# Optimization experiments

Hardware: AMD Instinct MI355X
Metric: run time of the kernel (lower is better)

The kernel has to match this reference:

```python
import jax, jax.numpy as jnp
import numpy as np

EMBED = 768
HEADS = 12
HEAD_DIM = EMBED // HEADS
HIDDEN = 4 * EMBED


def layer_norm(x, gamma, beta, eps=1e-5):
    mu = jnp.mean(x, axis=-1, keepdims=True)
    var = jnp.var(x, axis=-1, keepdims=True)
    return (x - mu) * jax.lax.rsqrt(var + eps) * gamma + beta


def setup_inputs() -> dict:
    key = jax.random.key(0)
    ks = jax.random.split(key, 10)
    B, N, C = 64, 577, EMBED
    s_in = 1.0 / np.sqrt(C)
    s_hid = 1.0 / np.sqrt(HIDDEN)
    return {
        "x": jax.random.normal(ks[0], (B, N, C), jnp.float32),
        "ln1_g": jnp.ones((C,), jnp.float32),
        "ln1_b": jnp.zeros((C,), jnp.float32),
        "w_qkv": jax.random.normal(ks[1], (C, 3 * C), jnp.float32) * s_in,  # no bias (qkv_bias=False)
        "w_proj": jax.random.normal(ks[2], (C, C), jnp.float32) * s_in,
        "b_proj": jnp.zeros((C,), jnp.float32),
        "ln2_g": jnp.ones((C,), jnp.float32),
        "ln2_b": jnp.zeros((C,), jnp.float32),
        "w_fc1": jax.random.normal(ks[3], (C, HIDDEN), jnp.float32) * s_in,
        "b_fc1": jnp.zeros((HIDDEN,), jnp.float32),
        "w_fc2": jax.random.normal(ks[4], (HIDDEN, C), jnp.float32) * s_hid,
        "b_fc2": jnp.zeros((C,), jnp.float32),
    }


def reference(x, ln1_g, ln1_b, w_qkv, w_proj, b_proj, ln2_g, ln2_b, w_fc1, b_fc1, w_fc2, b_fc2):
    B, N, C = x.shape
    # --- attention branch (pre-norm) ---
    h = layer_norm(x, ln1_g, ln1_b)
    qkv = (h @ w_qkv).reshape(B, N, 3, HEADS, HEAD_DIM)
    q = jnp.transpose(qkv[:, :, 0], (0, 2, 1, 3))  # [B,H,N,D]
    k = jnp.transpose(qkv[:, :, 1], (0, 2, 1, 3))
    v = jnp.transpose(qkv[:, :, 2], (0, 2, 1, 3))
    scale = HEAD_DIM ** -0.5
    att = jax.nn.softmax(jnp.einsum("bhnd,bhmd->bhnm", q, k) * scale, axis=-1)
    o = jnp.einsum("bhnm,bhmd->bhnd", att, v)
    o = jnp.transpose(o, (0, 2, 1, 3)).reshape(B, N, C)
    x = x + (o @ w_proj + b_proj)
    # --- MLP branch (pre-norm) ---
    h = layer_norm(x, ln2_g, ln2_b)
    h = jax.nn.gelu(h @ w_fc1 + b_fc1, approximate=False)
    x = x + (h @ w_fc2 + b_fc2)
    return x
```

## Files before the change

kernel.cpp:

```cpp
#include <hip/hip_runtime.h>
#include <hip/hip_bf16.h>
#include <math.h>

using bf16 = __hip_bfloat16;
typedef __attribute__((ext_vector_type(8))) short short8;
typedef __attribute__((ext_vector_type(4))) float f32x4;

#define NSEQ   577
#define NBATCH 64
#define NTOK   36928
#define MPAD   37120
#define NHEADS 12
#define HDIM   64
#define NP     640
#define CEMB   768
#define CHID   3072
#define NBH    (NBATCH*NHEADS)

__device__ __forceinline__ bf16 f2bf(float v){ return __float2bfloat16(v); }

__device__ __forceinline__ float gelu_f(float x) {
    float x3 = x * x * x;
    float y = 1.5957691216057308f * (x + 0.044715f * x3);
    float e = __expf(y);
    float t = 1.0f - 2.0f / (e + 1.0f);
    return 0.5f * x * (1.0f + t);
}

#define GLOAD_LDS16(gaddr, laddr) \
  __builtin_amdgcn_global_load_lds((__attribute__((address_space(1))) const void*)(gaddr), \
                                   (__attribute__((address_space(3))) void*)(laddr), 16, 0, 0)

__global__ __launch_bounds__(256) void transpose_w(const float* __restrict__ src,
                                                   bf16* __restrict__ dst, int R, int C) {
    long idx = (long)blockIdx.x * 256 + threadIdx.x;
    long total = (long)R * C;
    if (idx < total) {
        int r = (int)(idx / C);
        int c = (int)(idx - (long)r * C);
        dst[(long)c * R + r] = f2bf(src[idx]);
    }
}

__global__ __launch_bounds__(256) void ln_kernel(const float* __restrict__ x,
                                                 const float* __restrict__ gamma,
                                                 const float* __restrict__ beta,
                                                 bf16* __restrict__ out) {
    int row = blockIdx.x;
    const float* xr = x + (size_t)row * CEMB;
    int tid = threadIdx.x;
    float v0 = xr[tid], v1 = xr[tid + 256], v2 = xr[tid + 512];
    float s = v0 + v1 + v2;
    #pragma unroll
    for (int o = 32; o > 0; o >>= 1) s += __shfl_down(s, o);
    __shared__ float red[4];
    if ((tid & 63) == 0) red[tid >> 6] = s;
    __syncthreads();
    float mean = (red[0] + red[1] + red[2] + red[3]) * (1.0f / CEMB);
    float d0 = v0 - mean, d1 = v1 - mean, d2 = v2 - mean;
    float q = d0*d0 + d1*d1 + d2*d2;
    #pragma unroll
    for (int o = 32; o > 0; o >>= 1) q += __shfl_down(q, o);
    __shared__ float red2[4];
    if ((tid & 63) == 0) red2[tid >> 6] = q;
    __syncthreads();
    float var = (red2[0] + red2[1] + red2[2] + red2[3]) * (1.0f / CEMB);
    float rs = rsqrtf(var + 1e-5f);
    bf16* orow = out + (size_t)row * CEMB;
    orow[tid]       = f2bf(d0 * rs * gamma[tid]       + beta[tid]);
    orow[tid + 256] = f2bf(d1 * rs * gamma[tid + 256] + beta[tid + 256]);
    orow[tid + 512] = f2bf(d2 * rs * gamma[tid + 512] + beta[tid + 512]);
}

__global__ __launch_bounds__(256) void flash_attn(const bf16* __restrict__ qg,
                                                  const bf16* __restrict__ kg,
                                                  const bf16* __restrict__ vtg,
                                                  bf16* __restrict__ og) {
    const int tid = threadIdx.x, lane = tid & 63, w = tid >> 6;
    const int fr = lane & 15, fh = lane >> 4;
    const int bh = blockIdx.y;
    const int q0 = blockIdx.x * 128;
    const int wr = w * 32;

    __shared__ bf16 Ks[2][64 * 64];
    __shared__ bf16 Vs[2][64 * 64];
    __shared__ bf16 Ps[128 * 64];

    const bf16* qb = qg  + (size_t)bh * NP * HDIM;
    const bf16* kb = kg  + (size_t)bh * NP * HDIM;
    const bf16* vb = vtg + (size_t)bh * HDIM * NP;

    const int swz  = (fr & 7) << 3;
    const int scol = (((lane & 7) ^ (lane >> 3)) << 3);
    const int srow = lane >> 3;

    short8 qa[2][2];
    #pragma unroll
    for (int mi = 0; mi < 2; mi++)
        #pragma unroll
        for (int ks = 0; ks < 2; ks++)
            qa[mi][ks] = *reinterpret_cast<const short8*>(
                qb + (size_t)(q0 + wr + mi * 16 + fr) * HDIM + ks * 32 + fh * 8);
    #pragma unroll
    for (int mi = 0; mi < 2; mi++)
        #pragma unroll
        for (int ks = 0; ks < 2; ks++)
            asm volatile("" : "+v"(qa[mi][ks]));

    f32x4 od[2][4] = {};
    float m_run[2] = {-1e30f, -1e30f};
    float l_run[2] = {0.f, 0.f};

    auto stageKV = [&](int buf, int kb0) {
        GLOAD_LDS16(kb + (size_t)(kb0 + w * 8 + srow) * HDIM + scol,      Ks[buf] + w * 512);
        GLOAD_LDS16(kb + (size_t)(kb0 + 32 + w * 8 + srow) * HDIM + scol, Ks[buf] + 2048 + w * 512);
        GLOAD_LDS16(vb + (size_t)(w * 8 + srow) * NP + kb0 + scol,        Vs[buf] + w * 512);
        GLOAD_LDS16(vb + (size_t)(32 + w * 8 + srow) * NP + kb0 + scol,   Vs[buf] + 2048 + w * 512);
    };

    auto tileBody = [&](int buf, int kb0) {
        f32x4 sacc[2][4] = {};
        short8 kf[4][2];
        #pragma unroll
        for (int n = 0; n < 4; n++)
            #pragma unroll
            for (int ks = 0; ks < 2; ks++)
                kf[n][ks] = *reinterpret_cast<const short8*>(
                    &Ks[buf][(n * 16 + fr) * 64 + ((ks * 32 + fh * 8) ^ swz)]);
        __builtin_amdgcn_s_setprio(1);
        #pragma unroll
        for (int mi = 0; mi < 2; mi++)
            #pragma unroll
            for (int n = 0; n < 4; n++)
                #pragma unroll
                for (int ks = 0; ks < 2; ks++)
                    sacc[mi][n] = __builtin_amdgcn_mfma_f32_16x16x32_bf16(kf[n][ks], qa[mi][ks], sacc[mi][n], 0, 0, 0);
        __builtin_amdgcn_s_setprio(0);

        #pragma unroll
        for (int mi = 0; mi < 2; mi++) {
            float sv[4][4];
            float tm = -1e30f;
            #pragma unroll
            for (int n = 0; n < 4; n++)
                #pragma unroll
                for (int r = 0; r < 4; r++) {
                    int key = kb0 + n * 16 + fh * 4 + r;
                    float s = sacc[mi][n][r];
                    sv[n][r] = (key < NSEQ) ? s : -1e30f;
                    tm = fmaxf(tm, sv[n][r]);
                }
            tm = fmaxf(tm, __shfl_xor(tm, 16));
            tm = fmaxf(tm, __shfl_xor(tm, 32));
            float mo = m_run[mi];
            if (__any(tm - mo > 8.f)) {
                float mn = fmaxf(mo, tm);
                float sc = __expf(mo - mn);
                m_run[mi] = mn;
                l_run[mi] *= sc;
                #pragma unroll
                for (int r = 0; r < 4; r++) {
                    float s2 = __shfl(sc, fh * 4 + r);
                    #pragma unroll
                    for (int n2 = 0; n2 < 4; n2++) od[mi][n2][r] *= s2;
                }
                mo = mn;
            }
            float ps = 0.f;
            #pragma unroll
            for (int n = 0; n < 4; n++)
                #pragma unroll
                for (int r = 0; r < 4; r++) {
                    float e = __expf(sv[n][r] - mo);
                    sv[n][r] = e; ps += e;
                }
            ps += __shfl_xor(ps, 16);
            ps += __shfl_xor(ps, 32);
            l_run[mi] += ps;
            const int q = wr + mi * 16 + fr;
            char* prow = (char*)(Ps + q * 64);
            #pragma unroll
            for (int n = 0; n < 4; n++) {
                bf16 b0 = f2bf(sv[n][0]), b1 = f2bf(sv[n][1]);
                bf16 b2 = f2bf(sv[n][2]), b3 = f2bf(sv[n][3]);
                unsigned int lo = (unsigned int)*(unsigned short*)&b0 |
                                  ((unsigned int)*(unsigned short*)&b1 << 16);
                unsigned int hi = (unsigned int)*(unsigned short*)&b2 |
                                  ((unsigned int)*(unsigned short*)&b3 << 16);
                int chunk = (2 * n + (fh >> 1)) ^ (fr & 7);
                uint2 pk; pk.x = lo; pk.y = hi;
                *reinterpret_cast<uint2*>(prow + (chunk << 4) + ((fh & 1) << 3)) = pk;
            }
        }
        asm volatile("s_waitcnt lgkmcnt(0)" ::: "memory");
        __builtin_amdgcn_sched_barrier(0);

        short8 pa[2][2], vf[4][2];
        #pragma unroll
        for (int mi = 0; mi < 2; mi++)
            #pragma unroll
            for (int ks = 0; ks < 2; ks++)
                pa[mi][ks] = *reinterpret_cast<const short8*>(
                    &Ps[(wr + mi * 16 + fr) * 64 + ((ks * 32 + fh * 8) ^ swz)]);
        #pragma unroll
        for (int n2 = 0; n2 < 4; n2++)
            #pragma unroll
            for (int ks = 0; ks < 2; ks++)
                vf[n2][ks] = *reinterpret_cast<const short8*>(
                    &Vs[buf][(n2 * 16 + fr) * 64 + ((ks * 32 + fh * 8) ^ swz)]);
        __builtin_amdgcn_s_setprio(1);
        #pragma unroll
        for (int mi = 0; mi < 2; mi++)
            #pragma unroll
            for (int n2 = 0; n2 < 4; n2++)
                #pragma unroll
                for (int ks = 0; ks < 2; ks++)
                    od[mi][n2] = __builtin_amdgcn_mfma_f32_16x16x32_bf16(pa[mi][ks], vf[n2][ks], od[mi][n2], 0, 0, 0);
        __builtin_amdgcn_s_setprio(0);
    };

    stageKV(0, 0);
    stageKV(1, 64);
    for (int t = 0; t < 9; ++t) {
        asm volatile("s_waitcnt vmcnt(4)" ::: "memory");
        __builtin_amdgcn_s_barrier();
        tileBody(t & 1, t * 64);
        asm volatile("s_waitcnt lgkmcnt(0)" ::: "memory");
        __builtin_amdgcn_s_barrier();
        if (t + 2 < 10) stageKV(t & 1, (t + 2) * 64);
    }
    asm volatile("s_waitcnt vmcnt(0)" ::: "memory");
    __builtin_amdgcn_s_barrier();
    tileBody(1, 9 * 64);

    const int b = bh / NHEADS, hh = bh - b * NHEADS;
    #pragma unroll
    for (int mi = 0; mi < 2; mi++)
        #pragma unroll
        for (int r = 0; r < 4; r++) {
            float lv = __shfl(l_run[mi], fh * 4 + r);
            int qrow = q0 + wr + mi * 16 + fh * 4 + r;
            if (qrow < NSEQ) {
                float inv = 1.f / lv;
                #pragma unroll
                for (int n2 = 0; n2 < 4; n2++)
                    og[((size_t)(b * NSEQ + qrow)) * CEMB + hh * HDIM + n2 * 16 + fr] =
                        f2bf(od[mi][n2][r] * inv);
            }
        }
}

#define MODE_QKV  1
#define MODE_PROJ 3
#define MODE_FC1  4
#define MODE_FC2  5

struct GemmParams {
    const bf16* A;
    const bf16* Bt;
    int M, N, K;
    int Mreal;
    float* Cf;
    bf16* Cb;
    const float* bias;
    const float* resid;
    bf16* qb; bf16* kb; bf16* vtb;
};

template<int MODE>
__global__ __launch_bounds__(512, 2) void gemm256(GemmParams p) {
    __shared__ bf16 AsBuf[2][256 * 64];
    __shared__ bf16 BsBuf[2][256 * 64];
    const int tid  = threadIdx.x;
    const int lane = tid & 63;
    const int w    = tid >> 6;

    const int gx = gridDim.x, gy = gridDim.y;
    const int nwg = gx * gy;
    const int orig = blockIdx.y * gx + blockIdx.x;
    const int q8 = nwg >> 3, r8 = nwg & 7;
    const int xcd = orig & 7, oid = orig >> 3;
    const int lin2 = ((xcd < r8) ? xcd * (q8 + 1) : r8 * (q8 + 1) + (xcd - r8) * q8) + oid;
    const int bm = (lin2 / gy) * 256;
    const int bn = (lin2 % gy) * 256;

    const int Kd = p.K;
    const int wm = w >> 2, wn = w & 3;
    const int wr = wm * 128, wc = wn * 64;
    const int fr = lane & 15;
    const int fk = (lane >> 4) * 8;
    const int swz = (fr & 7) << 3;

    const int sr = w * 8 + (lane >> 3);
    const int scol = (((lane & 7) ^ (lane >> 3)) << 3);

    f32x4 acc[8][4] = {};

    auto stageS = [&](bf16* Ad, bf16* Bd, int kt, int s) {
        GLOAD_LDS16(p.A  + (size_t)(bm + s * 64 + sr) * Kd + (size_t)kt * 64 + scol,
                    Ad + (size_t)(s * 8 + w) * 512);
        GLOAD_LDS16(p.Bt + (size_t)(bn + s * 64 + sr) * Kd + (size_t)kt * 64 + scol,
                    Bd + (size_t)(s * 8 + w) * 512);
    };

    auto PHASE = [&](const bf16* Ad, const bf16* Bd, int ks, int mh,
                     bf16* An, bf16* Bn, int ktn, int s0, int s1, bool doStage) {
        short8 bfr[4], afr[4];
        #pragma unroll
        for (int n = 0; n < 4; n++)
            bfr[n] = *reinterpret_cast<const short8*>(
                &Bd[(wc + n * 16 + fr) * 64 + ((ks * 32 + fk) ^ swz)]);
        #pragma unroll
        for (int m = 0; m < 4; m++)
            afr[m] = *reinterpret_cast<const short8*>(
                &Ad[(wr + (mh * 4 + m) * 16 + fr) * 64 + ((ks * 32 + fk) ^ swz)]);
        if (doStage) { stageS(An, Bn, ktn, s0); stageS(An, Bn, ktn, s1); }
        __builtin_amdgcn_s_barrier();
        asm volatile("s_waitcnt lgkmcnt(0)" ::: "memory");
        __builtin_amdgcn_sched_barrier(0);
        __builtin_amdgcn_s_setprio(1);
        #pragma unroll
        for (int m = 0; m < 4; m++)
            #pragma unroll
            for (int n = 0; n < 4; n++)
                acc[mh * 4 + m][n] = __builtin_amdgcn_mfma_f32_16x16x32_bf16(
                    afr[m], bfr[n], acc[mh * 4 + m][n], 0, 0, 0);
        __builtin_amdgcn_s_setprio(0);
        __builtin_amdgcn_s_barrier();
    };

    const int T = Kd >> 6;
    stageS(AsBuf[0], BsBuf[0], 0, 0);
    stageS(AsBuf[0], BsBuf[0], 0, 1);
    stageS(AsBuf[0], BsBuf[0], 0, 2);
    stageS(AsBuf[0], BsBuf[0], 0, 3);
    asm volatile("s_waitcnt vmcnt(0)" ::: "memory");
    __builtin_amdgcn_s_barrier();

    for (int t = 0; t < T; ++t) {
        const bf16* Ad = AsBuf[t & 1]; const bf16* Bd = BsBuf[t & 1];
        bf16* An = AsBuf[(t + 1) & 1]; bf16* Bn = BsBuf[(t + 1) & 1];
        const bool st = (t + 1 < T);
        PHASE(Ad, Bd, 0, 0, An, Bn, t + 1, 0, 1, st);
        PHASE(Ad, Bd, 0, 1, An, Bn, t + 1, 2, 3, st);
        PHASE(Ad, Bd, 1, 0, An, Bn, 0, 0, 0, false);
        PHASE(Ad, Bd, 1, 1, An, Bn, 0, 0, 0, false);
        if (st) asm volatile("s_waitcnt vmcnt(0)" ::: "memory");
        __builtin_amdgcn_s_barrier();
    }

    const int fq = (lane >> 4) * 4;
    const int colw = bn + wc;

    if (MODE == MODE_QKV) {
        const int which = colw / CEMB;
        const int hh = (colw - which * CEMB) >> 6;
        const float scl = (which == 0) ? 0.125f : 1.0f;
        #pragma unroll
        for (int m = 0; m < 8; m++)
        #pragma unroll
        for (int r = 0; r < 4; r++) {
            int row = bm + wr + m * 16 + fq + r;
            if (row < p.Mreal) {
                int b2 = row / NSEQ;
                int n2 = row - b2 * NSEQ;
                size_t bh = (size_t)b2 * NHEADS + hh;
                if (which == 0) {
                    bf16* dst = p.qb + (bh * NP + n2) * HDIM + fr;
                    #pragma unroll
                    for (int n = 0; n < 4; n++) dst[n * 16] = f2bf(acc[m][n][r] * scl);
                } else if (which == 1) {
                    bf16* dst = p.kb + (bh * NP + n2) * HDIM + fr;
                    #pragma unroll
                    for (int n = 0; n < 4; n++) dst[n * 16] = f2bf(acc[m][n][r]);
                } else {
                    bf16* dst = p.vtb + (bh * HDIM + fr) * NP + n2;
                    #pragma unroll
                    for (int n = 0; n < 4; n++) dst[(size_t)n * 16 * NP] = f2bf(acc[m][n][r]);
                }
            }
        }
    } else if (MODE == MODE_FC1) {
        const float* bp = p.bias + colw + fr;
        float bb[4];
        #pragma unroll
        for (int n = 0; n < 4; n++) bb[n] = bp[n * 16];
        #pragma unroll
        for (int m = 0; m < 8; m++)
        #pragma unroll
        for (int r = 0; r < 4; r++) {
            int row = bm + wr + m * 16 + fq + r;
            if (row < p.Mreal) {
                bf16* crow = p.Cb + (size_t)row * p.N + colw + fr;
                #pragma unroll
                for (int n = 0; n < 4; n++)
                    crow[n * 16] = f2bf(gelu_f(acc[m][n][r] + bb[n]));
            }
        }
    } else {
        const float* bp = p.bias + colw + fr;
        float bb[4];
        #pragma unroll
        for (int n = 0; n < 4; n++) bb[n] = bp[n * 16];
        #pragma unroll
        for (int m = 0; m < 8; m++)
        #pragma unroll
        for (int r = 0; r < 4; r++) {
            int row = bm + wr + m * 16 + fq + r;
            if (row < p.Mreal) {
                float* crow = p.Cf + (size_t)row * p.N + colw + fr;
                const float* rrow = p.resid + (size_t)row * p.N + colw + fr;
                #pragma unroll
                for (int n = 0; n < 4; n++)
                    crow[n * 16] = acc[m][n][r] + bb[n] + rrow[n * 16];
            }
        }
    }
}

extern "C" void kernel_launch(void* const* d_in, const int* in_sizes, int n_in,
                              void* d_out, int out_size, void* d_ws, size_t ws_size,
                              hipStream_t stream) {
    const float* x      = (const float*)d_in[0];
    const float* ln1_g  = (const float*)d_in[1];
    const float* ln1_b  = (const float*)d_in[2];
    const float* w_qkv  = (const float*)d_in[3];
    const float* w_proj = (const float*)d_in[4];
    const float* b_proj = (const float*)d_in[5];
    const float* ln2_g  = (const float*)d_in[6];
    const float* ln2_b  = (const float*)d_in[7];
    const float* w_fc1  = (const float*)d_in[8];
    const float* b_fc1  = (const float*)d_in[9];
    const float* w_fc2  = (const float*)d_in[10];
    const float* b_fc2  = (const float*)d_in[11];
    float* out = (float*)d_out;

    char* ws = (char*)d_ws;
    auto al = [](size_t b){ return (b + 255) & ~(size_t)255; };
    size_t off = 0;
    auto take = [&](size_t b)->char* { char* p = ws + off; off += al(b); return p; };

    bf16* wqkvT  = (bf16*)take((size_t)2304 * 768 * 2);
    bf16* wprojT = (bf16*)take((size_t)768 * 768 * 2);
    bf16* wfc1T  = (bf16*)take((size_t)3072 * 768 * 2);
    bf16* wfc2T  = (bf16*)take((size_t)768 * 3072 * 2);
    bf16* h      = (bf16*)take((size_t)MPAD * CEMB * 2);
    bf16* o      = (bf16*)take((size_t)MPAD * CEMB * 2);
    size_t fixedEnd = off;

    const size_t qkvB = (size_t)NBH * NP * HDIM * 2;
    bf16* q_c  = (bf16*)(ws + fixedEnd);
    bf16* k_c  = (bf16*)(ws + fixedEnd + qkvB);
    bf16* vT_c = (bf16*)(ws + fixedEnd + 2 * qkvB);
    bf16* g_c  = (bf16*)(ws + fixedEnd);

    transpose_w<<<(768 * 2304 + 255) / 256, 256, 0, stream>>>(w_qkv, wqkvT, 768, 2304);
    transpose_w<<<(768 * 768 + 255) / 256, 256, 0, stream>>>(w_proj, wprojT, 768, 768);
    transpose_w<<<(768 * 3072 + 255) / 256, 256, 0, stream>>>(w_fc1, wfc1T, 768, 3072);
    transpose_w<<<(3072 * 768 + 255) / 256, 256, 0, stream>>>(w_fc2, wfc2T, 3072, 768);

    ln_kernel<<<NTOK, 256, 0, stream>>>(x, ln1_g, ln1_b, h);

    {
        GemmParams p{};
        p.A = h; p.Bt = wqkvT;
        p.M = MPAD; p.N = 3 * CEMB; p.K = CEMB; p.Mreal = NTOK;
        p.qb = q_c; p.kb = k_c; p.vtb = vT_c;
        gemm256<MODE_QKV><<<dim3(MPAD / 256, 3 * CEMB / 256), 512, 0, stream>>>(p);
    }

    flash_attn<<<dim3(NP / 128, NBH), 256, 0, stream>>>(q_c, k_c, vT_c, o);

    {
        GemmParams p{};
        p.A = o; p.Bt = wprojT;
        p.M = MPAD; p.N = CEMB; p.K = CEMB; p.Mreal = NTOK;
        p.Cf = out; p.bias = b_proj; p.resid = x;
        gemm256<MODE_PROJ><<<dim3(MPAD / 256, CEMB / 256), 512, 0, stream>>>(p);
    }

    ln_kernel<<<NTOK, 256, 0, stream>>>(out, ln2_g, ln2_b, h);

    {
        GemmParams p{};
        p.A = h; p.Bt = wfc1T;
        p.M = MPAD; p.N = CHID; p.K = CEMB; p.Mreal = NTOK;
        p.Cb = g_c; p.bias = b_fc1;
        gemm256<MODE_FC1><<<dim3(MPAD / 256, CHID / 256), 512, 0, stream>>>(p);
    }

    {
        GemmParams p{};
        p.A = g_c; p.Bt = wfc2T;
        p.M = MPAD; p.N = CEMB; p.K = CHID; p.Mreal = NTOK;
        p.Cf = out; p.bias = b_fc2; p.resid = out;
        gemm256<MODE_FC2><<<dim3(MPAD / 256, CEMB / 256), 512, 0, stream>>>(p);
    }
}
```

Baseline: 1.349 ms.

## Shrink GEMM tile to 256x128 and use triple-buffered LDS prefetch

The shared GEMM kernel now uses 256x128 output tiles instead of 256x256, and each wave owns a 64x64 sub-tile. Shared memory goes to three stages and global-to-LDS loads are issued two K-tiles ahead, with the wait relaxed to vmcnt(6), so loads overlap compute more deeply. Each wave keeps half as many accumulators and the grid has twice as many workgroups, which helps load balance and occupancy. In exchange, arithmetic intensity per tile drops and the A operand is re-read twice as often.

```diff
diff --git a/kernel.cpp b/kernel.cpp
--- a/kernel.cpp
+++ b/kernel.cpp
@@ -269,8 +269,8 @@
 
 template<int MODE>
 __global__ __launch_bounds__(512, 2) void gemm256(GemmParams p) {
-    __shared__ bf16 AsBuf[2][256 * 64];
-    __shared__ bf16 BsBuf[2][256 * 64];
+    __shared__ bf16 As[3][256 * 64];
+    __shared__ bf16 Bs[3][128 * 64];
     const int tid  = threadIdx.x;
     const int lane = tid & 63;
     const int w    = tid >> 6;
@@ -282,71 +282,73 @@
     const int xcd = orig & 7, oid = orig >> 3;
     const int lin2 = ((xcd < r8) ? xcd * (q8 + 1) : r8 * (q8 + 1) + (xcd - r8) * q8) + oid;
     const int bm = (lin2 / gy) * 256;
-    const int bn = (lin2 % gy) * 256;
+    const int bn = (lin2 % gy) * 128;
 
     const int Kd = p.K;
-    const int wm = w >> 2, wn = w & 3;
-    const int wr = wm * 128, wc = wn * 64;
+    const int wm = w >> 1, wn = w & 1;
+    const int wr = wm * 64, wc = wn * 64;
     const int fr = lane & 15;
     const int fk = (lane >> 4) * 8;
     const int swz = (fr & 7) << 3;
 
-    const int sr = w * 8 + (lane >> 3);
-    const int scol = (((lane & 7) ^ (lane >> 3)) << 3);
-
-    f32x4 acc[8][4] = {};
-
-    auto stageS = [&](bf16* Ad, bf16* Bd, int kt, int s) {
-        GLOAD_LDS16(p.A  + (size_t)(bm + s * 64 + sr) * Kd + (size_t)kt * 64 + scol,
-                    Ad + (size_t)(s * 8 + w) * 512);
-        GLOAD_LDS16(p.Bt + (size_t)(bn + s * 64 + sr) * Kd + (size_t)kt * 64 + scol,
-                    Bd + (size_t)(s * 8 + w) * 512);
+    const int row0 = tid >> 3;
+    const int scol = (((tid & 7) ^ ((tid >> 3) & 7)) << 3);
+    const bf16* aB[4]; const bf16* bB[2];
+    #pragma unroll
+    for (int j = 0; j < 4; j++) aB[j] = p.A  + (size_t)(bm + row0 + j * 64) * Kd + scol;
+    #pragma unroll
+    for (int j = 0; j < 2; j++) bB[j] = p.Bt + (size_t)(bn + row0 + j * 64) * Kd + scol;
+
+    f32x4 acc[4][4] = {};
+
+    auto stA = [&](int buf, int kt, int j) {
+        GLOAD_LDS16(aB[j] + (size_t)kt * 64, As[buf] + (size_t)(tid + j * 512) * 8);
     };
-
-    auto PHASE = [&](const bf16* Ad, const bf16* Bd, int ks, int mh,
-                     bf16* An, bf16* Bn, int ktn, int s0, int s1, bool doStage) {
-        short8 bfr[4], afr[4];
-        #pragma unroll
-        for (int n = 0; n < 4; n++)
-            bfr[n] = *reinterpret_cast<const short8*>(
-                &Bd[(wc + n * 16 + fr) * 64 + ((ks * 32 + fk) ^ swz)]);
-        #pragma unroll
-        for (int m = 0; m < 4; m++)
-            afr[m] = *reinterpret_cast<const short8*>(
-                &Ad[(wr + (mh * 4 + m) * 16 + fr) * 64 + ((ks * 32 + fk) ^ swz)]);
-        if (doStage) { stageS(An, Bn, ktn, s0); stageS(An, Bn, ktn, s1); }
+    auto stB = [&](int buf, int kt, int j) {
+        GLOAD_LDS16(bB[j] + (size_t)kt * 64, Bs[buf] + (size_t)(tid + j * 512) * 8);
+    };
+
+    const int T = Kd >> 6;
+    stA(0, 0, 0); stA(0, 0, 1); stA(0, 0, 2); stA(0, 0, 3); stB(0, 0, 0); stB(0, 0, 1);
+    stA(1, 1, 0); stA(1, 1, 1); stA(1, 1, 2); stA(1, 1, 3); stB(1, 1, 0); stB(1, 1, 1);
+
+    int cur = 0;
+    for (int t = 0; t < T; ++t) {
+        if (t + 1 < T) { asm volatile("s_waitcnt vmcnt(6)" ::: "memory"); }
+        else           { asm volatile("s_waitcnt vmcnt(0)" ::: "memory"); }
         __builtin_amdgcn_s_barrier();
-        asm volatile("s_waitcnt lgkmcnt(0)" ::: "memory");
-        __builtin_amdgcn_sched_barrier(0);
-        __builtin_amdgcn_s_setprio(1);
-        #pragma unroll
-        for (int m = 0; m < 4; m++)
+        int nb = cur + 2; if (nb >= 3) nb -= 3;
+        const bool st = (t + 2 < T);
+        const bf16* Ad = As[cur]; const bf16* Bd = Bs[cur];
+        #pragma unroll
+        for (int ks = 0; ks < 2; ks++) {
+            short8 afr[4], bfr[4];
             #pragma unroll
             for (int n = 0; n < 4; n++)
-                acc[mh * 4 + m][n] = __builtin_amdgcn_mfma_f32_16x16x32_bf16(
-                    afr[m], bfr[n], acc[mh * 4 + m][n], 0, 0, 0);
-        __builtin_amdgcn_s_setprio(0);
-        __builtin_amdgcn_s_barrier();
-    };
-
-    const int T = Kd >> 6;
-    stageS(AsBuf[0], BsBuf[0], 0, 0);
-    stageS(AsBuf[0], BsBuf[0], 0, 1);
-    stageS(AsBuf[0], BsBuf[0], 0, 2);
-    stageS(AsBuf[0], BsBuf[0], 0, 3);
-    asm volatile("s_waitcnt vmcnt(0)" ::: "memory");
-    __builtin_amdgcn_s_barrier();
-
-    for (int t = 0; t < T; ++t) {
-        const bf16* Ad = AsBuf[t & 1]; const bf16* Bd = BsBuf[t & 1];
-        bf16* An = AsBuf[(t + 1) & 1]; bf16* Bn = BsBuf[(t + 1) & 1];
-        const bool st = (t + 1 < T);
-        PHASE(Ad, Bd, 0, 0, An, Bn, t + 1, 0, 1, st);
-        PHASE(Ad, Bd, 0, 1, An, Bn, t + 1, 2, 3, st);
-        PHASE(Ad, Bd, 1, 0, An, Bn, 0, 0, 0, false);
-        PHASE(Ad, Bd, 1, 1, An, Bn, 0, 0, 0, false);
-        if (st) asm volatile("s_waitcnt vmcnt(0)" ::: "memory");
-        __builtin_amdgcn_s_barrier();
+                bfr[n] = *reinterpret_cast<const short8*>(
+                    &Bd[(wc + n * 16 + fr) * 64 + ((ks * 32 + fk) ^ swz)]);
+            #pragma unroll
+            for (int m = 0; m < 4; m++)
+                afr[m] = *reinterpret_cast<const short8*>(
+                    &Ad[(wr + m * 16 + fr) * 64 + ((ks * 32 + fk) ^ swz)]);
+            if (st) {
+                if (ks == 0) { stA(nb, t + 2, 0); stA(nb, t + 2, 1); stA(nb, t + 2, 2); }
+                else         { stA(nb, t + 2, 3); stB(nb, t + 2, 0); stB(nb, t + 2, 1); }
+            }
+            __builtin_amdgcn_s_barrier();
+            asm volatile("s_waitcnt lgkmcnt(0)" ::: "memory");
+            __builtin_amdgcn_sched_barrier(0);
+            __builtin_amdgcn_s_setprio(1);
+            #pragma unroll
+            for (int m = 0; m < 4; m++)
+                #pragma unroll
+                for (int n = 0; n < 4; n++)
+                    acc[m][n] = __builtin_amdgcn_mfma_f32_16x16x32_bf16(
+                        afr[m], bfr[n], acc[m][n], 0, 0, 0);
+            __builtin_amdgcn_s_setprio(0);
+            __builtin_amdgcn_s_barrier();
+        }
+        cur = (cur + 1 == 3) ? 0 : cur + 1;
     }
 
     const int fq = (lane >> 4) * 4;
@@ -357,7 +359,7 @@
         const int hh = (colw - which * CEMB) >> 6;
         const float scl = (which == 0) ? 0.125f : 1.0f;
         #pragma unroll
-        for (int m = 0; m < 8; m++)
+        for (int m = 0; m < 4; m++)
         #pragma unroll
         for (int r = 0; r < 4; r++) {
             int row = bm + wr + m * 16 + fq + r;
@@ -386,7 +388,7 @@
         #pragma unroll
         for (int n = 0; n < 4; n++) bb[n] = bp[n * 16];
         #pragma unroll
-        for (int m = 0; m < 8; m++)
+        for (int m = 0; m < 4; m++)
         #pragma unroll
         for (int r = 0; r < 4; r++) {
             int row = bm + wr + m * 16 + fq + r;
@@ -403,7 +405,7 @@
         #pragma unroll
         for (int n = 0; n < 4; n++) bb[n] = bp[n * 16];
         #pragma unroll
-        for (int m = 0; m < 8; m++)
+        for (int m = 0; m < 4; m++)
         #pragma unroll
         for (int r = 0; r < 4; r++) {
             int row = bm + wr + m * 16 + fq + r;
@@ -466,7 +468,7 @@
         p.A = h; p.Bt = wqkvT;
         p.M = MPAD; p.N = 3 * CEMB; p.K = CEMB; p.Mreal = NTOK;
         p.qb = q_c; p.kb = k_c; p.vtb = vT_c;
-        gemm256<MODE_QKV><<<dim3(MPAD / 256, 3 * CEMB / 256), 512, 0, stream>>>(p);
+        gemm256<MODE_QKV><<<dim3(MPAD / 256, 3 * CEMB / 128), 512, 0, stream>>>(p);
     }
 
     flash_attn<<<dim3(NP / 128, NBH), 256, 0, stream>>>(q_c, k_c, vT_c, o);
@@ -476,7 +478,7 @@
         p.A = o; p.Bt = wprojT;
         p.M = MPAD; p.N = CEMB; p.K = CEMB; p.Mreal = NTOK;
         p.Cf = out; p.bias = b_proj; p.resid = x;
-        gemm256<MODE_PROJ><<<dim3(MPAD / 256, CEMB / 256), 512, 0, stream>>>(p);
+        gemm256<MODE_PROJ><<<dim3(MPAD / 256, CEMB / 128), 512, 0, stream>>>(p);
     }
 
     ln_kernel<<<NTOK, 256, 0, stream>>>(out, ln2_g, ln2_b, h);
@@ -486,7 +488,7 @@
         p.A = h; p.Bt = wfc1T;
         p.M = MPAD; p.N = CHID; p.K = CEMB; p.Mreal = NTOK;
         p.Cb = g_c; p.bias = b_fc1;
-        gemm256<MODE_FC1><<<dim3(MPAD / 256, CHID / 256), 512, 0, stream>>>(p);
+        gemm256<MODE_FC1><<<dim3(MPAD / 256, CHID / 128), 512, 0, stream>>>(p);
     }
 
     {
@@ -494,6 +496,6 @@
         p.A = g_c; p.Bt = wfc2T;
         p.M = MPAD; p.N = CEMB; p.K = CHID; p.Mreal = NTOK;
         p.Cf = out; p.bias = b_fc2; p.resid = out;
-        gemm256<MODE_FC2><<<dim3(MPAD / 256, CEMB / 256), 512, 0, stream>>>(p);
+        gemm256<MODE_FC2><<<dim3(MPAD / 256, CEMB / 128), 512, 0, stream>>>(p);
     }
 }
```

New measurement: 1.372 ms. No clear change (+1.8%).
